# Kernel optimization log

Hardware: AMD Instinct MI355X
Metric: run time of the kernel (lower is better)

Reference implementation:

```python
import jax, jax.numpy as jnp
import numpy as np

F_NUM, D_IN, D_OUT, H = 64, 256, 256, 8
LN_EPS = 1e-5


def setup_inputs() -> dict:
    key = jax.random.key(0)
    ks = jax.random.split(key, 7)
    B = 1024
    dh = D_OUT // H
    # xavier_normal_ with gain 1.414 on [F, d, w]: std = gain*sqrt(2/(fan_in+fan_out)),
    # torch treats dim0 as batch-of-matrices only for 2D; for 3D fan_in=d*w? Use simple
    # gaussian init scaled like xavier over the last two dims (values irrelevant to math).
    std_qkv = 1.414 * np.sqrt(2.0 / (D_IN + D_OUT))
    std_lin = 1.414 * np.sqrt(2.0 / (D_IN + D_OUT))
    std_w = 1.414 * np.sqrt(2.0 / (1 + dh))
    return {
        "theta": jax.random.normal(ks[0], (B, F_NUM, D_IN), jnp.float32),
        "Q": jax.random.normal(ks[1], (F_NUM, D_IN, D_OUT), jnp.float32) * std_qkv,
        "K": jax.random.normal(ks[2], (F_NUM, D_IN, D_OUT), jnp.float32) * std_qkv,
        "V": jax.random.normal(ks[3], (F_NUM, D_IN, D_OUT), jnp.float32) * std_qkv,
        "W_lin": jax.random.normal(ks[4], (D_OUT, D_IN), jnp.float32) * std_lin,  # Linear weight [out,in]
        "rot_w": jax.random.normal(ks[5], (1, dh), jnp.float32) * std_w,
        "ln_gamma": jnp.ones((D_OUT,), jnp.float32),
        "ln_beta": jnp.zeros((D_OUT,), jnp.float32),
    }


def _split_heads(x, H):
    B, F, W = x.shape
    return x.reshape(B, F, H, W // H).transpose(0, 2, 1, 3)  # [B,H,F,dh]


def reference(theta, Q, K, V, W_lin, rot_w, ln_gamma, ln_beta):
    B = theta.shape[0]
    t = theta.reshape(B, -1, D_IN)  # [B,F,d]
    q = jnp.einsum('bfd,fdw->bfw', t, Q)
    k = jnp.einsum('bfd,fdw->bfw', t, K)
    v = jnp.einsum('bfd,fdw->bfw', t, V)
    q, k, v = _split_heads(q, H), _split_heads(k, H), _split_heads(v, H)  # [B,H,F,dh]
    cos_a = jnp.cos(q) * rot_w
    sin_a = jnp.sin(q) * rot_w
    logits = (jnp.einsum('bhfe,bhge->bhfg', cos_a, jnp.cos(k))
              + jnp.einsum('bhfe,bhge->bhfg', sin_a, jnp.sin(k)))
    S = jax.nn.sigmoid(logits)  # [B,H,F,F] (query f, key g)
    # (dropout p=0 -> identity)
    out = jnp.einsum('bhfg,bhgd->bhfd', S, v)  # [B,H,F,dh]
    out = out.transpose(0, 2, 1, 3).reshape(B, F_NUM, D_OUT)  # concat heads in order
    res = out + jnp.einsum('bfd,wd->bfw', theta, W_lin)
    mu = jnp.mean(res, axis=-1, keepdims=True)
    var = jnp.mean((res - mu) ** 2, axis=-1, keepdims=True)
    normed = (res - mu) * jax.lax.rsqrt(var + LN_EPS)
    return normed * ln_gamma + ln_beta
```

## Files before the change

kernel.cpp:

```cpp
#include <hip/hip_runtime.h>

typedef __attribute__((ext_vector_type(8))) short bf16x8;
typedef __attribute__((ext_vector_type(8))) unsigned short u16x8;
typedef __attribute__((ext_vector_type(4))) unsigned short u16x4;
typedef __attribute__((ext_vector_type(4))) float f32x4;
typedef unsigned short u16;

__device__ __forceinline__ float b2f(u16 u) {
    return __builtin_bit_cast(float, (unsigned)u << 16);
}
__device__ __forceinline__ u16 f2b(float f) {
    unsigned i = __builtin_bit_cast(unsigned, f);
    return (u16)((i + 0x7FFFu + ((i >> 16) & 1u)) >> 16);
}
__device__ __forceinline__ void async_cp16(const u16* g, u16* l) {
    __builtin_amdgcn_global_load_lds((const __attribute__((address_space(1))) void*)g,
                                     (__attribute__((address_space(3))) void*)l, 16, 0, 0);
}

__global__ __launch_bounds__(256) void wtrans_kernel(
    const float* __restrict__ Q, const float* __restrict__ K, const float* __restrict__ V,
    u16* __restrict__ WT)
{
    int z = blockIdx.z; int m = z >> 6, f = z & 63;
    const float* src = (m == 0 ? Q : (m == 1 ? K : V)) + (size_t)f * 65536;
    u16* dst = WT + (size_t)z * 65536;
    int w0 = blockIdx.x * 64, d0 = blockIdx.y * 64;
    __shared__ u16 tile[64][68];
    int tid = threadIdx.x;
#pragma unroll
    for (int i = 0; i < 2; ++i) {
        int idx = tid * 2 + i; int r = idx >> 3; int c8 = (idx & 7) * 8;
        const float* p = src + (size_t)(d0 + r) * 256 + w0 + c8;
        f32x4 a = *(const f32x4*)p, b = *(const f32x4*)(p + 4);
        u16x4 lo, hi;
#pragma unroll
        for (int j = 0; j < 4; ++j) { lo[j] = f2b(a[j]); hi[j] = f2b(b[j]); }
        *(u16x4*)&tile[r][c8] = lo;
        *(u16x4*)&tile[r][c8 + 4] = hi;
    }
    __syncthreads();
#pragma unroll
    for (int i = 0; i < 2; ++i) {
        int idx = tid * 2 + i; int rw = idx >> 3; int c8 = (idx & 7) * 8;
        u16x8 v;
#pragma unroll
        for (int j = 0; j < 8; ++j) v[j] = tile[c8 + j][rw];
        *(u16x8*)(dst + (size_t)(w0 + rw) * 256 + d0 + c8) = v;
    }
}

__global__ __launch_bounds__(256, 2) void qkv_gemm_kernel(
    const float* __restrict__ theta, const u16* __restrict__ WT, u16* __restrict__ ws, int B)
{
    int f = blockIdx.z;
    int bm0 = blockIdx.x * 128, bn0 = blockIdx.y * 128;
    __shared__ u16 smem[32768];
    int tid = threadIdx.x, wave = tid >> 6, lane = tid & 63;
    int l15 = lane & 15, quad = lane >> 4;
    int wm0 = (wave >> 1) * 64, wn0 = (wave & 1) * 64;

    const float* Af = theta + (size_t)f * 256;
#pragma unroll
    for (int p = 0; p < 16; ++p) {
        int id = p * 256 + tid;
        int r = id >> 5, c = id & 31;
        const float* g = Af + (size_t)(bm0 + r) * 16384 + c * 8;
        f32x4 a = *(const f32x4*)g, b = *(const f32x4*)(g + 4);
        u16x8 v;
#pragma unroll
        for (int j = 0; j < 4; ++j) { v[j] = f2b(a[j]); v[j + 4] = f2b(b[j]); }
        *(u16x8*)&smem[r * 256 + ((c ^ (r & 7)) * 8)] = v;
    }
    __syncthreads();
    bf16x8 af[4][8];
#pragma unroll
    for (int mi = 0; mi < 4; ++mi)
#pragma unroll
        for (int kk = 0; kk < 8; ++kk) {
            int row = wm0 + mi * 16 + l15;
            int pos = (kk * 4 + quad) ^ (l15 & 7);
            af[mi][kk] = *(const bf16x8*)&smem[row * 256 + pos * 8];
        }
    __syncthreads();

    auto issueB = [&](int it) {
        int m = it >> 3, kk = it & 7, buf = it & 1;
        const u16* Bt = WT + (size_t)(m * 64 + f) * 65536;
#pragma unroll
        for (int i = 0; i < 2; ++i) {
            int r0 = wave * 32 + i * 16;
            const u16* g = Bt + (size_t)(bn0 + r0 + (lane >> 2)) * 256 + kk * 32 + (lane & 3) * 8;
            async_cp16(g, &smem[buf * 4096 + r0 * 32]);
        }
    };
    issueB(0);
    f32x4 acc[4][4];
#pragma unroll
    for (int it = 0; it < 24; ++it) {
        int kk = it & 7, buf = it & 1;
        if (kk == 0) {
#pragma unroll
            for (int mi = 0; mi < 4; ++mi)
#pragma unroll
                for (int ni = 0; ni < 4; ++ni) acc[mi][ni] = f32x4{0.f, 0.f, 0.f, 0.f};
        }
        __syncthreads();
        if (it < 23) issueB(it + 1);
        bf16x8 bfr[4];
#pragma unroll
        for (int ni = 0; ni < 4; ++ni)
            bfr[ni] = *(const bf16x8*)&smem[buf * 4096 + (wn0 + ni * 16 + l15) * 32 + quad * 8];
#pragma unroll
        for (int mi = 0; mi < 4; ++mi)
#pragma unroll
            for (int ni = 0; ni < 4; ++ni)
                acc[mi][ni] = __builtin_amdgcn_mfma_f32_16x16x32_bf16(af[mi][kk], bfr[ni], acc[mi][ni], 0, 0, 0);
        if (kk == 7) {
            int m = it >> 3;
            u16* C = ws + (size_t)m * B * 16384 + (size_t)f * 256;
#pragma unroll
            for (int mi = 0; mi < 4; ++mi)
#pragma unroll
                for (int ni = 0; ni < 4; ++ni)
#pragma unroll
                    for (int r = 0; r < 4; ++r)
                        C[(size_t)(bm0 + wm0 + mi * 16 + quad * 4 + r) * 16384 + bn0 + wn0 + ni * 16 + l15] =
                            f2b(acc[mi][ni][r]);
        }
    }
}

__global__ __launch_bounds__(256) void attn_kernel(
    const u16* __restrict__ qws, const u16* __restrict__ kws, const u16* __restrict__ vws,
    float* __restrict__ attf, const float* __restrict__ rotw)
{
    int b = blockIdx.x;
    int tid = threadIdx.x, wave = tid >> 6, lane = tid & 63;
    int l15 = lane & 15, quad = lane >> 4;
    __shared__ u16 Sb[4][64][72];
    __shared__ u16 Vb[4][64][32];
    const size_t base = (size_t)b * (64 * 256);
    float rw[8];
    {
        f32x4 r0 = *(const f32x4*)(rotw + quad * 8);
        f32x4 r1 = *(const f32x4*)(rotw + quad * 8 + 4);
#pragma unroll
        for (int j = 0; j < 4; ++j) { rw[j] = r0[j]; rw[j + 4] = r1[j]; }
    }
    for (int hi = 0; hi < 2; ++hi) {
        int h = wave + hi * 4;
        const u16* qh = qws + base + h * 32;
        const u16* kh = kws + base + h * 32;
        const u16* vh = vws + base + h * 32;
#pragma unroll
        for (int i = 0; i < 4; ++i) {
            int row = i * 16 + (lane >> 2); int c8 = (lane & 3) * 8;
            *(u16x8*)&Vb[wave][row][c8] = *(const u16x8*)(vh + (size_t)row * 256 + c8);
        }
        bf16x8 af[4][2], bfr[4][2];
#pragma unroll
        for (int mi = 0; mi < 4; ++mi) {
            u16x8 q8 = *(const u16x8*)(qh + (size_t)(mi * 16 + l15) * 256 + quad * 8);
            bf16x8 c, s;
#pragma unroll
            for (int j = 0; j < 8; ++j) {
                float v = b2f(q8[j]);
                c[j] = (short)f2b(__cosf(v) * rw[j]);
                s[j] = (short)f2b(__sinf(v) * rw[j]);
            }
            af[mi][0] = c; af[mi][1] = s;
        }
#pragma unroll
        for (int ni = 0; ni < 4; ++ni) {
            u16x8 k8 = *(const u16x8*)(kh + (size_t)(ni * 16 + l15) * 256 + quad * 8);
            bf16x8 c, s;
#pragma unroll
            for (int j = 0; j < 8; ++j) {
                float v = b2f(k8[j]);
                c[j] = (short)f2b(__cosf(v));
                s[j] = (short)f2b(__sinf(v));
            }
            bfr[ni][0] = c; bfr[ni][1] = s;
        }
        f32x4 acc[4][4];
#pragma unroll
        for (int mi = 0; mi < 4; ++mi)
#pragma unroll
            for (int ni = 0; ni < 4; ++ni) acc[mi][ni] = f32x4{0.f, 0.f, 0.f, 0.f};
#pragma unroll
        for (int kc = 0; kc < 2; ++kc)
#pragma unroll
            for (int mi = 0; mi < 4; ++mi)
#pragma unroll
                for (int ni = 0; ni < 4; ++ni)
                    acc[mi][ni] = __builtin_amdgcn_mfma_f32_16x16x32_bf16(af[mi][kc], bfr[ni][kc], acc[mi][ni], 0, 0, 0);
#pragma unroll
        for (int mi = 0; mi < 4; ++mi)
#pragma unroll
            for (int ni = 0; ni < 4; ++ni)
#pragma unroll
                for (int r = 0; r < 4; ++r) {
                    float x = acc[mi][ni][r];
                    float sg = __builtin_amdgcn_rcpf(1.f + __expf(-x));
                    Sb[wave][mi * 16 + quad * 4 + r][ni * 16 + l15] = f2b(sg);
                }
        f32x4 ao[4][2];
#pragma unroll
        for (int mi = 0; mi < 4; ++mi)
#pragma unroll
            for (int n2 = 0; n2 < 2; ++n2) ao[mi][n2] = f32x4{0.f, 0.f, 0.f, 0.f};
#pragma unroll
        for (int kc = 0; kc < 2; ++kc) {
            bf16x8 pb[2];
#pragma unroll
            for (int n2 = 0; n2 < 2; ++n2)
#pragma unroll
                for (int j = 0; j < 8; ++j)
                    pb[n2][j] = (short)Vb[wave][kc * 32 + quad * 8 + j][n2 * 16 + l15];
#pragma unroll
            for (int mi = 0; mi < 4; ++mi) {
                bf16x8 pa = *(const bf16x8*)&Sb[wave][mi * 16 + l15][kc * 32 + quad * 8];
#pragma unroll
                for (int n2 = 0; n2 < 2; ++n2)
                    ao[mi][n2] = __builtin_amdgcn_mfma_f32_16x16x32_bf16(pa, pb[n2], ao[mi][n2], 0, 0, 0);
            }
        }
#pragma unroll
        for (int mi = 0; mi < 4; ++mi)
#pragma unroll
            for (int n2 = 0; n2 < 2; ++n2)
#pragma unroll
                for (int r = 0; r < 4; ++r)
                    attf[base + (size_t)(mi * 16 + quad * 4 + r) * 256 + h * 32 + n2 * 16 + l15] =
                        ao[mi][n2][r];
    }
}

__global__ __launch_bounds__(512) void lin_ln_kernel(
    const float* __restrict__ theta, const float* __restrict__ Wl, const float* att,
    const float* __restrict__ gamma, const float* __restrict__ beta, float* out)
{
    int tid = threadIdx.x, wave = tid >> 6, lane = tid & 63;
    int l15 = lane & 15, quad = lane >> 4;
    int bm0 = blockIdx.x * 128;
    int wm0 = (wave >> 2) * 64, wn0 = (wave & 3) * 64;
    int wn = wave & 3;
    __shared__ u16 As[128][32];
    __shared__ u16 Bs[256][32];
    __shared__ float red1[128][4];
    __shared__ float red2[128][4];
    f32x4 acc[4][4];
#pragma unroll
    for (int mi = 0; mi < 4; ++mi)
#pragma unroll
        for (int ni = 0; ni < 4; ++ni) acc[mi][ni] = f32x4{0.f, 0.f, 0.f, 0.f};
    for (int k0 = 0; k0 < 256; k0 += 32) {
        {
            int r = tid >> 2; int c8 = (tid & 3) * 8;
            const float* p = theta + (size_t)(bm0 + r) * 256 + k0 + c8;
            f32x4 a = *(const f32x4*)p, b = *(const f32x4*)(p + 4);
            u16x8 v;
#pragma unroll
            for (int j = 0; j < 4; ++j) { v[j] = f2b(a[j]); v[j + 4] = f2b(b[j]); }
            *(u16x8*)&As[r][c8] = v;
        }
#pragma unroll
        for (int i = 0; i < 2; ++i) {
            int idx = tid * 2 + i; int r = idx >> 2; int c8 = (idx & 3) * 8;
            const float* p = Wl + (size_t)r * 256 + k0 + c8;
            f32x4 a = *(const f32x4*)p, b = *(const f32x4*)(p + 4);
            u16x8 v;
#pragma unroll
            for (int j = 0; j < 4; ++j) { v[j] = f2b(a[j]); v[j + 4] = f2b(b[j]); }
            *(u16x8*)&Bs[r][c8] = v;
        }
        __syncthreads();
        bf16x8 af[4], bfr[4];
#pragma unroll
        for (int mi = 0; mi < 4; ++mi) af[mi] = *(const bf16x8*)&As[wm0 + mi * 16 + l15][quad * 8];
#pragma unroll
        for (int ni = 0; ni < 4; ++ni) bfr[ni] = *(const bf16x8*)&Bs[wn0 + ni * 16 + l15][quad * 8];
#pragma unroll
        for (int mi = 0; mi < 4; ++mi)
#pragma unroll
            for (int ni = 0; ni < 4; ++ni)
                acc[mi][ni] = __builtin_amdgcn_mfma_f32_16x16x32_bf16(af[mi], bfr[ni], acc[mi][ni], 0, 0, 0);
        __syncthreads();
    }
    float gam[4], bet[4];
#pragma unroll
    for (int ni = 0; ni < 4; ++ni) {
        gam[ni] = gamma[wn0 + ni * 16 + l15];
        bet[ni] = beta[wn0 + ni * 16 + l15];
    }
#pragma unroll
    for (int mi = 0; mi < 4; ++mi)
#pragma unroll
        for (int ni = 0; ni < 4; ++ni)
#pragma unroll
            for (int r = 0; r < 4; ++r)
                acc[mi][ni][r] += att[(size_t)(bm0 + wm0 + mi * 16 + quad * 4 + r) * 256 + wn0 + ni * 16 + l15];
#pragma unroll
    for (int mi = 0; mi < 4; ++mi)
#pragma unroll
        for (int r = 0; r < 4; ++r) {
            float s1 = 0.f, s2 = 0.f;
#pragma unroll
            for (int ni = 0; ni < 4; ++ni) { float x = acc[mi][ni][r]; s1 += x; s2 += x * x; }
#pragma unroll
            for (int off = 1; off < 16; off <<= 1) {
                s1 += __shfl_xor(s1, off);
                s2 += __shfl_xor(s2, off);
            }
            if (l15 == 0) {
                int lr = wm0 + mi * 16 + quad * 4 + r;
                red1[lr][wn] = s1; red2[lr][wn] = s2;
            }
        }
    __syncthreads();
#pragma unroll
    for (int mi = 0; mi < 4; ++mi)
#pragma unroll
        for (int r = 0; r < 4; ++r) {
            int lr = wm0 + mi * 16 + quad * 4 + r;
            float s1 = red1[lr][0] + red1[lr][1] + red1[lr][2] + red1[lr][3];
            float s2 = red2[lr][0] + red2[lr][1] + red2[lr][2] + red2[lr][3];
            float mu = s1 * (1.f / 256.f);
            float var = s2 * (1.f / 256.f) - mu * mu;
            float inv = rsqrtf(var + 1e-5f);
#pragma unroll
            for (int ni = 0; ni < 4; ++ni) {
                float y = (acc[mi][ni][r] - mu) * inv * gam[ni] + bet[ni];
                out[(size_t)(bm0 + lr) * 256 + wn0 + ni * 16 + l15] = y;
            }
        }
}

extern "C" void kernel_launch(void* const* d_in, const int* in_sizes, int n_in,
                              void* d_out, int out_size, void* d_ws, size_t ws_size,
                              hipStream_t stream)
{
    const float* theta = (const float*)d_in[0];
    const float* Q  = (const float*)d_in[1];
    const float* K  = (const float*)d_in[2];
    const float* V  = (const float*)d_in[3];
    const float* Wl = (const float*)d_in[4];
    const float* rotw = (const float*)d_in[5];
    const float* gam = (const float*)d_in[6];
    const float* bet = (const float*)d_in[7];
    int B = in_sizes[0] / (64 * 256);
    u16* ws = (u16*)d_ws;
    size_t per = (size_t)B * 16384;
    u16* wsq = ws;
    u16* wsk = ws + per;
    u16* wsv = ws + 2 * per;
    u16* wT  = ws + 3 * per;
    float* outf = (float*)d_out;

    wtrans_kernel<<<dim3(4, 4, 192), 256, 0, stream>>>(Q, K, V, wT);
    qkv_gemm_kernel<<<dim3(B / 128, 2, 64), 256, 0, stream>>>(theta, wT, ws, B);
    attn_kernel<<<dim3(B), 256, 0, stream>>>(wsq, wsk, wsv, outf, rotw);
    lin_ln_kernel<<<dim3(B * 64 / 128), 512, 0, stream>>>(theta, Wl, outf, gam, bet, outf);
}
```

Baseline: 289.9 us.

## Pre-convert W_lin to bf16, drop LDS staging for B operands, use hardware trig/exp

The weight-transpose kernel gets an extra z-slice that converts W_lin to bf16 once. The linear+LayerNorm kernel then stages the whole theta tile in swizzled LDS and reads W_lin bf16 fragments straight from global, with no per-k-step syncs. The QKV GEMM drops its async double-buffered LDS pipeline for B and loads fragments directly from global/L2. The attention kernel switches to native amdgcn sin/cos with a 1/2π prescale and exp2-based sigmoid, and bf16 packing is done in pairs. The direct global loads can cost more latency than the removed syncs save, and the native trig may lose accuracy for large arguments.

```diff
diff --git a/kernel.cpp b/kernel.cpp
--- a/kernel.cpp
+++ b/kernel.cpp
@@ -13,29 +13,44 @@
     unsigned i = __builtin_bit_cast(unsigned, f);
     return (u16)((i + 0x7FFFu + ((i >> 16) & 1u)) >> 16);
 }
-__device__ __forceinline__ void async_cp16(const u16* g, u16* l) {
-    __builtin_amdgcn_global_load_lds((const __attribute__((address_space(1))) void*)g,
-                                     (__attribute__((address_space(3))) void*)l, 16, 0, 0);
+__device__ __forceinline__ unsigned pkb(float a, float b) {
+    return (unsigned)f2b(a) | ((unsigned)f2b(b) << 16);
 }
 
 __global__ __launch_bounds__(256) void wtrans_kernel(
     const float* __restrict__ Q, const float* __restrict__ K, const float* __restrict__ V,
-    u16* __restrict__ WT)
-{
-    int z = blockIdx.z; int m = z >> 6, f = z & 63;
+    const float* __restrict__ Wl, u16* __restrict__ WT, u16* __restrict__ WlB)
+{
+    int z = blockIdx.z;
+    int tid = threadIdx.x;
+    if (z == 192) {
+        int w0 = blockIdx.x * 64, d0 = blockIdx.y * 64;
+#pragma unroll
+        for (int i = 0; i < 2; ++i) {
+            int idx = tid * 2 + i; int r = idx >> 3; int c8 = (idx & 7) * 8;
+            const float* p = Wl + (size_t)(w0 + r) * 256 + d0 + c8;
+            f32x4 a = *(const f32x4*)p, b = *(const f32x4*)(p + 4);
+            u16x8 v;
+            ((unsigned*)&v)[0] = pkb(a[0], a[1]); ((unsigned*)&v)[1] = pkb(a[2], a[3]);
+            ((unsigned*)&v)[2] = pkb(b[0], b[1]); ((unsigned*)&v)[3] = pkb(b[2], b[3]);
+            *(u16x8*)(WlB + (size_t)(w0 + r) * 256 + d0 + c8) = v;
+        }
+        return;
+    }
+    if (z > 192) return;
+    int m = z >> 6, f = z & 63;
     const float* src = (m == 0 ? Q : (m == 1 ? K : V)) + (size_t)f * 65536;
     u16* dst = WT + (size_t)z * 65536;
     int w0 = blockIdx.x * 64, d0 = blockIdx.y * 64;
     __shared__ u16 tile[64][68];
-    int tid = threadIdx.x;
 #pragma unroll
     for (int i = 0; i < 2; ++i) {
         int idx = tid * 2 + i; int r = idx >> 3; int c8 = (idx & 7) * 8;
         const float* p = src + (size_t)(d0 + r) * 256 + w0 + c8;
         f32x4 a = *(const f32x4*)p, b = *(const f32x4*)(p + 4);
         u16x4 lo, hi;
-#pragma unroll
-        for (int j = 0; j < 4; ++j) { lo[j] = f2b(a[j]); hi[j] = f2b(b[j]); }
+        ((unsigned*)&lo)[0] = pkb(a[0], a[1]); ((unsigned*)&lo)[1] = pkb(a[2], a[3]);
+        ((unsigned*)&hi)[0] = pkb(b[0], b[1]); ((unsigned*)&hi)[1] = pkb(b[2], b[3]);
         *(u16x4*)&tile[r][c8] = lo;
         *(u16x4*)&tile[r][c8 + 4] = hi;
     }
@@ -55,7 +70,7 @@
 {
     int f = blockIdx.z;
     int bm0 = blockIdx.x * 128, bn0 = blockIdx.y * 128;
-    __shared__ u16 smem[32768];
+    __shared__ u16 smem[128 * 256];
     int tid = threadIdx.x, wave = tid >> 6, lane = tid & 63;
     int l15 = lane & 15, quad = lane >> 4;
     int wm0 = (wave >> 1) * 64, wn0 = (wave & 1) * 64;
@@ -68,8 +83,8 @@
         const float* g = Af + (size_t)(bm0 + r) * 16384 + c * 8;
         f32x4 a = *(const f32x4*)g, b = *(const f32x4*)(g + 4);
         u16x8 v;
-#pragma unroll
-        for (int j = 0; j < 4; ++j) { v[j] = f2b(a[j]); v[j + 4] = f2b(b[j]); }
+        ((unsigned*)&v)[0] = pkb(a[0], a[1]); ((unsigned*)&v)[1] = pkb(a[2], a[3]);
+        ((unsigned*)&v)[2] = pkb(b[0], b[1]); ((unsigned*)&v)[3] = pkb(b[2], b[3]);
         *(u16x8*)&smem[r * 256 + ((c ^ (r & 7)) * 8)] = v;
     }
     __syncthreads();
@@ -82,52 +97,35 @@
             int pos = (kk * 4 + quad) ^ (l15 & 7);
             af[mi][kk] = *(const bf16x8*)&smem[row * 256 + pos * 8];
         }
-    __syncthreads();
-
-    auto issueB = [&](int it) {
-        int m = it >> 3, kk = it & 7, buf = it & 1;
-        const u16* Bt = WT + (size_t)(m * 64 + f) * 65536;
-#pragma unroll
-        for (int i = 0; i < 2; ++i) {
-            int r0 = wave * 32 + i * 16;
-            const u16* g = Bt + (size_t)(bn0 + r0 + (lane >> 2)) * 256 + kk * 32 + (lane & 3) * 8;
-            async_cp16(g, &smem[buf * 4096 + r0 * 32]);
-        }
-    };
-    issueB(0);
+
     f32x4 acc[4][4];
-#pragma unroll
-    for (int it = 0; it < 24; ++it) {
-        int kk = it & 7, buf = it & 1;
-        if (kk == 0) {
+    for (int m = 0; m < 3; ++m) {
+        const u16* Bt = WT + (size_t)(m * 64 + f) * 65536 + (size_t)(bn0 + wn0) * 256;
+#pragma unroll
+        for (int mi = 0; mi < 4; ++mi)
+#pragma unroll
+            for (int ni = 0; ni < 4; ++ni) acc[mi][ni] = f32x4{0.f, 0.f, 0.f, 0.f};
+#pragma unroll
+        for (int kk = 0; kk < 8; ++kk) {
+            bf16x8 bfr[4];
+#pragma unroll
+            for (int ni = 0; ni < 4; ++ni)
+                bfr[ni] = *(const bf16x8*)(Bt + (size_t)(ni * 16 + l15) * 256 + kk * 32 + quad * 8);
 #pragma unroll
             for (int mi = 0; mi < 4; ++mi)
 #pragma unroll
-                for (int ni = 0; ni < 4; ++ni) acc[mi][ni] = f32x4{0.f, 0.f, 0.f, 0.f};
-        }
-        __syncthreads();
-        if (it < 23) issueB(it + 1);
-        bf16x8 bfr[4];
-#pragma unroll
-        for (int ni = 0; ni < 4; ++ni)
-            bfr[ni] = *(const bf16x8*)&smem[buf * 4096 + (wn0 + ni * 16 + l15) * 32 + quad * 8];
+                for (int ni = 0; ni < 4; ++ni)
+                    acc[mi][ni] = __builtin_amdgcn_mfma_f32_16x16x32_bf16(af[mi][kk], bfr[ni], acc[mi][ni], 0, 0, 0);
+        }
+        u16* C = ws + (size_t)m * B * 16384 + (size_t)f * 256;
 #pragma unroll
         for (int mi = 0; mi < 4; ++mi)
 #pragma unroll
             for (int ni = 0; ni < 4; ++ni)
-                acc[mi][ni] = __builtin_amdgcn_mfma_f32_16x16x32_bf16(af[mi][kk], bfr[ni], acc[mi][ni], 0, 0, 0);
-        if (kk == 7) {
-            int m = it >> 3;
-            u16* C = ws + (size_t)m * B * 16384 + (size_t)f * 256;
-#pragma unroll
-            for (int mi = 0; mi < 4; ++mi)
-#pragma unroll
-                for (int ni = 0; ni < 4; ++ni)
-#pragma unroll
-                    for (int r = 0; r < 4; ++r)
-                        C[(size_t)(bm0 + wm0 + mi * 16 + quad * 4 + r) * 16384 + bn0 + wn0 + ni * 16 + l15] =
-                            f2b(acc[mi][ni][r]);
-        }
+#pragma unroll
+                for (int r = 0; r < 4; ++r)
+                    C[(size_t)(bm0 + wm0 + mi * 16 + quad * 4 + r) * 16384 + bn0 + wn0 + ni * 16 + l15] =
+                        f2b(acc[mi][ni][r]);
     }
 }
 
@@ -135,6 +133,8 @@
     const u16* __restrict__ qws, const u16* __restrict__ kws, const u16* __restrict__ vws,
     float* __restrict__ attf, const float* __restrict__ rotw)
 {
+    constexpr float INV2PI = 0.15915494309189535f;
+    constexpr float LOG2E = 1.4426950408889634f;
     int b = blockIdx.x;
     int tid = threadIdx.x, wave = tid >> 6, lane = tid & 63;
     int l15 = lane & 15, quad = lane >> 4;
@@ -162,26 +162,40 @@
 #pragma unroll
         for (int mi = 0; mi < 4; ++mi) {
             u16x8 q8 = *(const u16x8*)(qh + (size_t)(mi * 16 + l15) * 256 + quad * 8);
-            bf16x8 c, s;
+            float cq[8], sq[8];
 #pragma unroll
             for (int j = 0; j < 8; ++j) {
-                float v = b2f(q8[j]);
-                c[j] = (short)f2b(__cosf(v) * rw[j]);
-                s[j] = (short)f2b(__sinf(v) * rw[j]);
-            }
-            af[mi][0] = c; af[mi][1] = s;
+                float v = b2f(q8[j]) * INV2PI;
+                cq[j] = __builtin_amdgcn_cosf(v);
+                sq[j] = __builtin_amdgcn_sinf(v);
+            }
+            u16x8 cv, sv;
+#pragma unroll
+            for (int j2 = 0; j2 < 4; ++j2) {
+                ((unsigned*)&cv)[j2] = pkb(cq[2 * j2] * rw[2 * j2], cq[2 * j2 + 1] * rw[2 * j2 + 1]);
+                ((unsigned*)&sv)[j2] = pkb(sq[2 * j2] * rw[2 * j2], sq[2 * j2 + 1] * rw[2 * j2 + 1]);
+            }
+            af[mi][0] = __builtin_bit_cast(bf16x8, cv);
+            af[mi][1] = __builtin_bit_cast(bf16x8, sv);
         }
 #pragma unroll
         for (int ni = 0; ni < 4; ++ni) {
             u16x8 k8 = *(const u16x8*)(kh + (size_t)(ni * 16 + l15) * 256 + quad * 8);
-            bf16x8 c, s;
+            float ck[8], sk[8];
 #pragma unroll
             for (int j = 0; j < 8; ++j) {
-                float v = b2f(k8[j]);
-                c[j] = (short)f2b(__cosf(v));
-                s[j] = (short)f2b(__sinf(v));
-            }
-            bfr[ni][0] = c; bfr[ni][1] = s;
+                float v = b2f(k8[j]) * INV2PI;
+                ck[j] = __builtin_amdgcn_cosf(v);
+                sk[j] = __builtin_amdgcn_sinf(v);
+            }
+            u16x8 cv, sv;
+#pragma unroll
+            for (int j2 = 0; j2 < 4; ++j2) {
+                ((unsigned*)&cv)[j2] = pkb(ck[2 * j2], ck[2 * j2 + 1]);
+                ((unsigned*)&sv)[j2] = pkb(sk[2 * j2], sk[2 * j2 + 1]);
+            }
+            bfr[ni][0] = __builtin_bit_cast(bf16x8, cv);
+            bfr[ni][1] = __builtin_bit_cast(bf16x8, sv);
         }
         f32x4 acc[4][4];
 #pragma unroll
@@ -202,7 +216,7 @@
 #pragma unroll
                 for (int r = 0; r < 4; ++r) {
                     float x = acc[mi][ni][r];
-                    float sg = __builtin_amdgcn_rcpf(1.f + __expf(-x));
+                    float sg = __builtin_amdgcn_rcpf(1.f + __builtin_amdgcn_exp2f(-LOG2E * x));
                     Sb[wave][mi * 16 + quad * 4 + r][ni * 16 + l15] = f2b(sg);
                 }
         f32x4 ao[4][2];
@@ -237,8 +251,8 @@
     }
 }
 
-__global__ __launch_bounds__(512) void lin_ln_kernel(
-    const float* __restrict__ theta, const float* __restrict__ Wl, const float* att,
+__global__ __launch_bounds__(512, 4) void lin_ln_kernel(
+    const float* __restrict__ theta, const u16* __restrict__ WlB, const float* att,
     const float* __restrict__ gamma, const float* __restrict__ beta, float* out)
 {
     int tid = threadIdx.x, wave = tid >> 6, lane = tid & 63;
@@ -246,47 +260,43 @@
     int bm0 = blockIdx.x * 128;
     int wm0 = (wave >> 2) * 64, wn0 = (wave & 3) * 64;
     int wn = wave & 3;
-    __shared__ u16 As[128][32];
-    __shared__ u16 Bs[256][32];
+    __shared__ u16 smem[128 * 256];
     __shared__ float red1[128][4];
     __shared__ float red2[128][4];
+#pragma unroll
+    for (int p = 0; p < 8; ++p) {
+        int id = p * 512 + tid;
+        int r = id >> 5, c = id & 31;
+        const float* g = theta + (size_t)(bm0 + r) * 256 + c * 8;
+        f32x4 a = *(const f32x4*)g, b = *(const f32x4*)(g + 4);
+        u16x8 v;
+        ((unsigned*)&v)[0] = pkb(a[0], a[1]); ((unsigned*)&v)[1] = pkb(a[2], a[3]);
+        ((unsigned*)&v)[2] = pkb(b[0], b[1]); ((unsigned*)&v)[3] = pkb(b[2], b[3]);
+        *(u16x8*)&smem[r * 256 + ((c ^ (r & 7)) * 8)] = v;
+    }
+    __syncthreads();
     f32x4 acc[4][4];
 #pragma unroll
     for (int mi = 0; mi < 4; ++mi)
 #pragma unroll
         for (int ni = 0; ni < 4; ++ni) acc[mi][ni] = f32x4{0.f, 0.f, 0.f, 0.f};
-    for (int k0 = 0; k0 < 256; k0 += 32) {
-        {
-            int r = tid >> 2; int c8 = (tid & 3) * 8;
-            const float* p = theta + (size_t)(bm0 + r) * 256 + k0 + c8;
-            f32x4 a = *(const f32x4*)p, b = *(const f32x4*)(p + 4);
-            u16x8 v;
-#pragma unroll
-            for (int j = 0; j < 4; ++j) { v[j] = f2b(a[j]); v[j + 4] = f2b(b[j]); }
-            *(u16x8*)&As[r][c8] = v;
-        }
-#pragma unroll
-        for (int i = 0; i < 2; ++i) {
-            int idx = tid * 2 + i; int r = idx >> 2; int c8 = (idx & 3) * 8;
-            const float* p = Wl + (size_t)r * 256 + k0 + c8;
-            f32x4 a = *(const f32x4*)p, b = *(const f32x4*)(p + 4);
-            u16x8 v;
-#pragma unroll
-            for (int j = 0; j < 4; ++j) { v[j] = f2b(a[j]); v[j + 4] = f2b(b[j]); }
-            *(u16x8*)&Bs[r][c8] = v;
-        }
-        __syncthreads();
+#pragma unroll
+    for (int kk = 0; kk < 8; ++kk) {
         bf16x8 af[4], bfr[4];
 #pragma unroll
-        for (int mi = 0; mi < 4; ++mi) af[mi] = *(const bf16x8*)&As[wm0 + mi * 16 + l15][quad * 8];
-#pragma unroll
-        for (int ni = 0; ni < 4; ++ni) bfr[ni] = *(const bf16x8*)&Bs[wn0 + ni * 16 + l15][quad * 8];
+        for (int mi = 0; mi < 4; ++mi) {
+            int row = wm0 + mi * 16 + l15;
+            int pos = (kk * 4 + quad) ^ (l15 & 7);
+            af[mi] = *(const bf16x8*)&smem[row * 256 + pos * 8];
+        }
+#pragma unroll
+        for (int ni = 0; ni < 4; ++ni)
+            bfr[ni] = *(const bf16x8*)(WlB + (size_t)(wn0 + ni * 16 + l15) * 256 + kk * 32 + quad * 8);
 #pragma unroll
         for (int mi = 0; mi < 4; ++mi)
 #pragma unroll
             for (int ni = 0; ni < 4; ++ni)
                 acc[mi][ni] = __builtin_amdgcn_mfma_f32_16x16x32_bf16(af[mi], bfr[ni], acc[mi][ni], 0, 0, 0);
-        __syncthreads();
     }
     float gam[4], bet[4];
 #pragma unroll
@@ -356,10 +366,11 @@
     u16* wsk = ws + per;
     u16* wsv = ws + 2 * per;
     u16* wT  = ws + 3 * per;
+    u16* wlb = wT + (size_t)192 * 65536;
     float* outf = (float*)d_out;
 
-    wtrans_kernel<<<dim3(4, 4, 192), 256, 0, stream>>>(Q, K, V, wT);
+    wtrans_kernel<<<dim3(4, 4, 193), 256, 0, stream>>>(Q, K, V, Wl, wT, wlb);
     qkv_gemm_kernel<<<dim3(B / 128, 2, 64), 256, 0, stream>>>(theta, wT, ws, B);
     attn_kernel<<<dim3(B), 256, 0, stream>>>(wsq, wsk, wsv, outf, rotw);
-    lin_ln_kernel<<<dim3(B * 64 / 128), 512, 0, stream>>>(theta, Wl, outf, gam, bet, outf);
-}
+    lin_ln_kernel<<<dim3(B * 64 / 128), 512, 0, stream>>>(theta, wlb, outf, gam, bet, outf);
+}
```

New measurement: 325.1 us. +12.1%, slower.
